# Kernel tuning notes

Measured on AMD Instinct MI355X. Metric: run time of the kernel, lower is better.

Reference implementation:

```python
import jax, jax.numpy as jnp
import numpy as np

B, N, C = 64, 8192, 64
C4 = C // 4
EPS_BN = 1e-5


def setup_inputs() -> dict:
    key = jax.random.key(0)
    ks = jax.random.split(key, 12)
    s = 0.05
    return {
        "x": jax.random.normal(ks[0], (B, N, 10), jnp.float32),
        "y": jax.random.normal(ks[1], (B, N, 13), jnp.float32),
        "W_l": jax.random.normal(ks[2], (10, C), jnp.float32) * s,
        "b_l": jax.random.normal(ks[3], (C,), jnp.float32) * s,
        "W_r": jax.random.normal(ks[4], (13, C), jnp.float32) * s,
        "b_r": jax.random.normal(ks[5], (C,), jnp.float32) * s,
        "W_qk": jax.random.normal(ks[6], (C4, C), jnp.float32) * s,  # shared q/k 1x1-conv weight
        "W_v": jax.random.normal(ks[7], (C, C), jnp.float32) * s,
        "b_v": jax.random.normal(ks[8], (C,), jnp.float32) * s,
        "W_t": jax.random.normal(ks[9], (C, C), jnp.float32) * s,
        "b_t": jax.random.normal(ks[10], (C,), jnp.float32) * s,
        "gamma": jnp.ones((C,), jnp.float32),
        "beta": jnp.zeros((C,), jnp.float32),
    }


def reference(x, y, W_l, b_l, W_r, b_r, W_qk, W_v, b_v, W_t, b_t, gamma, beta):
    # x: [B,N,10] -> linear_l; y: [B,N,13] -> linear_r  (torch keeps [B,C,N]; we keep [B,N,C])
    X = x @ W_l + b_l                                   # [B,N,C]
    Y = y @ W_r + b_r                                   # [B,N,C]
    # 1x1 convs == per-point matmuls; attention runs ACROSS the batch dim per point n
    xq = jnp.einsum('bnc,dc->nbd', X, W_qk)             # [N,B,C/4]
    yk = jnp.einsum('bnc,dc->nbd', Y, W_qk)             # [N,B,C/4] (shared weight)
    yv = jnp.einsum('bnc,dc->nbd', Y, W_v) + b_v        # [N,B,C]
    energy = jnp.einsum('nbd,ned->nbe', xq, yk)         # [N,B,B]
    attn = jax.nn.softmax(energy, axis=-1)
    # extra L1 renormalization over dim=1 (offset-attention style)
    attn = attn / (1e-9 + attn.sum(axis=1, keepdims=True))
    yr = jnp.einsum('nbe,nec->bnc', attn, yv)           # [B,N,C]
    # trans_conv -> BatchNorm (training-mode batch stats) -> ReLU -> residual -> max over points
    t = jnp.einsum('bnc,dc->bnd', X - yr, W_t) + b_t    # [B,N,C]
    mean = t.mean(axis=(0, 1))
    var = t.var(axis=(0, 1))                            # biased var, as BN uses
    tn = gamma * (t - mean) * jax.lax.rsqrt(var + EPS_BN) + beta
    xres = X + jax.nn.relu(tn)                          # [B,N,C]
    return jnp.max(xres, axis=1)[:, :, None]            # [B,C,1] to match torch layout
```

## Files before the change

### kernel.cpp

```cpp
#include <hip/hip_runtime.h>

#define B_ 64
#define N_ 8192

using short8 = __attribute__((ext_vector_type(8))) short;
using f32x4  = __attribute__((ext_vector_type(4))) float;

#define MFMA16(a, b, c) __builtin_amdgcn_mfma_f32_16x16x32_bf16((a), (b), (c), 0, 0, 0)

__device__ inline unsigned short f2bf(float f) {
  union { float f; unsigned int u; } v; v.f = f;
  return (unsigned short)((v.u + 0x8000u) >> 16);
}
__device__ inline float bf2f(unsigned int hi16_in_low) {
  union { unsigned int u; float f; } v; v.u = hi16_in_low << 16;
  return v.f;
}
__device__ inline unsigned u2(float a, float b) {
  return (unsigned)f2bf(a) | ((unsigned)f2bf(b) << 16);
}
__device__ inline void put_y(short* Ar0, short* YT0, int b, int f, unsigned short h) {
  const int s = (f >= 13) ? 1 : 0;
  Ar0[16 + f + 2547 * s] = (short)h;
  YT0[f * 72 + b + 216 * s] = (short)h;
}


__global__ void k0_prep(const float* __restrict__ W_l, const float* __restrict__ b_l,
                        const float* __restrict__ W_r, const float* __restrict__ b_r,
                        const float* __restrict__ W_qk, const float* __restrict__ W_v,
                        const float* __restrict__ b_v, const float* __restrict__ W_t,
                        float* __restrict__ wsf) {
  const int tid = threadIdx.x;
  unsigned short* wb   = (unsigned short*)(wsf + 66688);
  unsigned short* BM   = wb;
  unsigned short* BL   = wb + 512;
  unsigned short* BRV2 = wb + 2560;
  unsigned short* BT   = wb + 4608;
  if (blockIdx.x == 0) {
    __shared__ float Wlq[11 * 16], Wrk[14 * 16];
    for (int idx = tid; idx < 11 * 16; idx += 256) {
      int i = idx >> 4, d = idx & 15;
      const float* a = (i < 10) ? (W_l + i * 64) : b_l;
      float s = 0.f;
      for (int c = 0; c < 64; ++c) s = fmaf(a[c], W_qk[d * 64 + c], s);
      Wlq[idx] = s;
    }
    for (int idx = tid; idx < 14 * 16; idx += 256) {
      int j = idx >> 4, d = idx & 15;
      const float* a = (j < 13) ? (W_r + j * 64) : b_r;
      float s = 0.f;
      for (int c = 0; c < 64; ++c) s = fmaf(a[c], W_qk[d * 64 + c], s);
      Wrk[idx] = s;
    }
    __syncthreads();
    for (int idx = tid; idx < 512; idx += 256) {
      int j = idx >> 5, kk = idx & 31;
      unsigned short o = 0;
      if (j < 14 && kk < 11) {
        float s = 0.f;
        for (int d = 0; d < 16; ++d) s = fmaf(Wlq[kk * 16 + d], Wrk[j * 16 + d], s);
        o = f2bf(s);
      }
      BM[idx] = o;
    }
  } else if (blockIdx.x == 1) {
    for (int idx = tid; idx < 2048; idx += 256) {
      int c = idx >> 5, kk = idx & 31;
      unsigned short o = 0;
      if (kk < 13) {
        float s = 0.f;
        for (int j = 0; j < 64; ++j) s = fmaf(W_r[kk * 64 + j], W_v[c * 64 + j], s);
        o = f2bf(s);
      } else if (kk == 13) {
        float s = b_v[c];
        for (int j = 0; j < 64; ++j) s = fmaf(b_r[j], W_v[c * 64 + j], s);
        o = f2bf(s);
      }
      BRV2[idx] = o;
    }
  } else if (blockIdx.x == 2) {
    for (int idx = tid; idx < 2048; idx += 256) {
      int c = idx >> 5, kk = idx & 31;
      unsigned short o = 0;
      if (kk < 10) o = f2bf(W_l[kk * 64 + c]);
      else if (kk == 10) o = f2bf(b_l[c]);
      BL[idx] = o;
    }
    for (int i = tid; i < 1024; i += 256) wsf[i] = 0.f;
  } else {
    for (int i = tid; i < 4096; i += 256) BT[i] = f2bf(W_t[i]);
  }
}

__global__ __launch_bounds__(256, 4)
void k1_attn(const float* __restrict__ x, const float* __restrict__ y,
             const float* __restrict__ wsf, const float* __restrict__ b_t,
             float* __restrict__ stats) {
  __shared__ __align__(16) short lds[19712];
  float* const statsScr = (float*)lds;
  short* const Axy[2] = {lds, lds + 2560};
  short* const YTb[2] = {lds + 5120, lds + 6272};
  short* const awB    = lds + 7424;
  short* const guB    = lds + 16640;
  float* const csF    = (float*)(lds + 18688);

  const unsigned short* wb   = (const unsigned short*)(wsf + 66688);
  const unsigned short* BM   = wb;
  const unsigned short* BL   = wb + 512;
  const unsigned short* BRV2 = wb + 2560;
  const unsigned short* BT   = wb + 4608;
  unsigned short* tg = (unsigned short*)(wsf + 66688) + 8704;

  const int tid  = threadIdx.x;
  const int w    = tid >> 6;
  const int lane = tid & 63;
  const int l15  = lane & 15;
  const int q    = lane >> 4;
  const int r0   = w * 16;
  const int n0   = blockIdx.x * 2;
  short* const aw[2] = {awB + w * 1152, awB + (4 + w) * 1152};
  short* const gu[2] = {guB + w * 256,  guB + (4 + w) * 256};

  {
    const int b = tid >> 2, i = tid & 3;
    const float* xb = x + ((size_t)b * N_ + n0) * 10;
    const float* yb = y + ((size_t)b * N_ + n0) * 13;
    short* const Ar0 = Axy[0] + b * 40;
    short* const Ar1 = Axy[1] + b * 40;
    short* const YT0 = YTb[0];
    {
      const float4 v = *(const float4*)(xb + 4 * i);
      const int g0 = 4 * i, g1 = 4 * i + 2;
      *(unsigned*)(Ar0 + (g0 >= 10 ? g0 + 2550 : g0)) = u2(v.x, v.y);
      *(unsigned*)(Ar0 + (g1 >= 10 ? g1 + 2550 : g1)) = u2(v.z, v.w);
      if (i == 0) {
        const float4 vv = *(const float4*)(xb + 16);
        *(unsigned*)(Ar1 + 6) = u2(vv.x, vv.y);
        *(unsigned*)(Ar1 + 8) = u2(vv.z, vv.w);
      }
    }
    if (i == 1) { *(unsigned*)(Ar1 + 10) = 0x3F80u; *(unsigned*)(Ar1 + 12) = 0u; *(unsigned*)(Ar1 + 14) = 0u; }
    if (i == 2) { *(unsigned*)(Ar0 + 10) = 0x3F80u; *(unsigned*)(Ar0 + 12) = 0u; *(unsigned*)(Ar0 + 14) = 0u; }
#pragma unroll
    for (int t = 0; t < 3; ++t) {
      const int j = i + 4 * t;
      const float2 v = *(const float2*)(yb + 2 * j);
      put_y(Ar0, YT0, b, 2 * j,     f2bf(v.x));
      put_y(Ar0, YT0, b, 2 * j + 1, f2bf(v.y));
    }
    if (i == 0) {
      const float2 v = *(const float2*)(yb + 24);
      put_y(Ar0, YT0, b, 24, f2bf(v.x));
      put_y(Ar0, YT0, b, 25, f2bf(v.y));
    }
    if (i == 3) {
      Ar0[29] = (short)0x3F80; *(unsigned*)(Ar0 + 30) = 0u;
      YT0[13 * 72 + b] = (short)0x3F80; YT0[14 * 72 + b] = 0; YT0[15 * 72 + b] = 0;
    }
    if (i == 2) {
      Ar1[29] = (short)0x3F80; *(unsigned*)(Ar1 + 30) = 0u;
      short* YT1 = YT0 + 1152;
      YT1[13 * 72 + b] = (short)0x3F80; YT1[14 * 72 + b] = 0; YT1[15 * 72 + b] = 0;
    }
  }
  asm volatile("s_waitcnt lgkmcnt(0)" ::: "memory");
  __builtin_amdgcn_sched_barrier(0);

  const short8 z8 = {0, 0, 0, 0, 0, 0, 0, 0};
  const f32x4 zero4 = {0.f, 0.f, 0.f, 0.f};

  const short8 bmF = *(const short8*)&BM[l15 * 32 + q * 8];
  short8 blF[4];
#pragma unroll
  for (int f = 0; f < 4; ++f) blF[f] = *(const short8*)&BL[(f * 16 + l15) * 32 + q * 8];

  f32x4 X[2][4];
  __builtin_amdgcn_s_setprio(1);
#pragma unroll
  for (int p = 0; p < 2; ++p) {
    const short8 aA = *(const short8*)&Axy[p][(r0 + l15) * 40 + q * 8];
    f32x4 G = MFMA16(aA, bmF, zero4);
#pragma unroll
    for (int f = 0; f < 4; ++f) X[p][f] = MFMA16(aA, blF[f], zero4);
#pragma unroll
    for (int j = 0; j < 4; ++j) gu[p][(q * 4 + j) * 16 + l15] = (short)f2bf(G[j]);
  }
  __builtin_amdgcn_s_setprio(0);
  __syncthreads();

  f32x4 E[2][4];
  __builtin_amdgcn_s_setprio(1);
#pragma unroll
  for (int p = 0; p < 2; ++p) {
    short8 aG = z8;
    if (q < 2) aG = *(const short8*)&gu[p][l15 * 16 + q * 8];
#pragma unroll
    for (int f = 0; f < 4; ++f) {
      short8 bk = z8;
      if (q < 2) bk = *(const short8*)&Axy[p][(f * 16 + l15) * 40 + 16 + q * 8];
      E[p][f] = MFMA16(aG, bk, zero4);
    }
  }
  __builtin_amdgcn_s_setprio(0);

  float inv_r[2][4];
#pragma unroll
  for (int p = 0; p < 2; ++p)
#pragma unroll
    for (int j = 0; j < 4; ++j) {
      float s = 0.f;
#pragma unroll
      for (int f = 0; f < 4; ++f) { E[p][f][j] = __expf(E[p][f][j]); s += E[p][f][j]; }
      s += __shfl_xor(s, 1);
      s += __shfl_xor(s, 2);
      s += __shfl_xor(s, 4);
      s += __shfl_xor(s, 8);
      inv_r[p][j] = 1.0f / s;
    }
#pragma unroll
  for (int p = 0; p < 2; ++p)
#pragma unroll
    for (int f = 0; f < 4; ++f) {
      float cs = E[p][f][0] * inv_r[p][0] + E[p][f][1] * inv_r[p][1] +
                 E[p][f][2] * inv_r[p][2] + E[p][f][3] * inv_r[p][3];
      cs += __shfl_xor(cs, 16);
      cs += __shfl_xor(cs, 32);
      if (lane < 16) csF[p * 256 + w * 64 + f * 16 + l15] = cs;
    }
  __syncthreads();

#pragma unroll
  for (int p = 0; p < 2; ++p) {
#pragma unroll
    for (int f = 0; f < 4; ++f) {
      const int col = f * 16 + l15;
      const float* sp = csF + p * 256;
      const float csv = 1.0f / (1e-9f + sp[col] + sp[64 + col] + sp[128 + col] + sp[192 + col]);
#pragma unroll
      for (int j = 0; j < 4; ++j)
        aw[p][(q * 4 + j) * 72 + col] = (short)f2bf(E[p][f][j] * inv_r[p][j] * csv);
    }
  }

  short8 brvF[4];
#pragma unroll
  for (int f = 0; f < 4; ++f) brvF[f] = *(const short8*)&BRV2[(f * 16 + l15) * 32 + q * 8];
  __builtin_amdgcn_s_setprio(1);
#pragma unroll
  for (int p = 0; p < 2; ++p) {
    const short8 aA0 = *(const short8*)&aw[p][l15 * 72 + q * 8];
    const short8 aA1 = *(const short8*)&aw[p][l15 * 72 + 32 + q * 8];
    f32x4 U = MFMA16(aA0, *(const short8*)&YTb[p][l15 * 72 + q * 8], zero4);
    U = MFMA16(aA1, *(const short8*)&YTb[p][l15 * 72 + 32 + q * 8], U);
#pragma unroll
    for (int j = 0; j < 4; ++j) gu[p][(q * 4 + j) * 16 + l15] = (short)f2bf(U[j]);
    short8 aU = z8;
    if (q < 2) aU = *(const short8*)&gu[p][l15 * 16 + q * 8];
#pragma unroll
    for (int f = 0; f < 4; ++f) {
      f32x4 yr = MFMA16(aU, brvF[f], zero4);
#pragma unroll
      for (int j = 0; j < 4; ++j)
        aw[p][(q * 4 + j) * 72 + f * 16 + l15] = (short)f2bf(X[p][f][j] - yr[j]);
    }
  }
  __builtin_amdgcn_s_setprio(0);

  float sRed[2][4], ssRed[2][4];
  uint2 pk[2][4];
  float4 btv[4];
  short8 btF0[4], btF1[4];
#pragma unroll
  for (int f = 0; f < 4; ++f) {
    btv[f] = *(const float4*)&b_t[f * 16 + q * 4];
    const int c = f * 16 + l15;
    btF0[f] = *(const short8*)&BT[c * 64 + q * 8];
    btF1[f] = *(const short8*)&BT[c * 64 + 32 + q * 8];
  }
  __builtin_amdgcn_s_setprio(1);
#pragma unroll
  for (int p = 0; p < 2; ++p) {
    const short8 aZ0 = *(const short8*)&aw[p][l15 * 72 + q * 8];
    const short8 aZ1 = *(const short8*)&aw[p][l15 * 72 + 32 + q * 8];
#pragma unroll
    for (int f = 0; f < 4; ++f) {
      const int c = f * 16 + l15;
      const float bT = b_t[c];
      f32x4 t = MFMA16(aZ0, btF0[f], ((f32x4){bT, bT, bT, bT}));
      t = MFMA16(aZ1, btF1[f], t);
      float s = 0.f, ss = 0.f;
#pragma unroll
      for (int j = 0; j < 4; ++j) { s += t[j]; ss = fmaf(t[j], t[j], ss); }
      s  += __shfl_xor(s, 16);  s  += __shfl_xor(s, 32);
      ss += __shfl_xor(ss, 16); ss += __shfl_xor(ss, 32);
      sRed[p][f] = s; ssRed[p][f] = ss;
      f32x4 tc = MFMA16(btF0[f], aZ0, ((f32x4){btv[f].x, btv[f].y, btv[f].z, btv[f].w}));
      tc = MFMA16(btF1[f], aZ1, tc);
      pk[p][f].x = (unsigned)f2bf(tc[0]) | ((unsigned)f2bf(tc[1]) << 16);
      pk[p][f].y = (unsigned)f2bf(tc[2]) | ((unsigned)f2bf(tc[3]) << 16);
    }
  }
  __builtin_amdgcn_s_setprio(0);
#pragma unroll
  for (int p = 0; p < 2; ++p)
#pragma unroll
    for (int f = 0; f < 4; ++f)
      *(uint2*)&tg[(size_t)(n0 + p) * 4096 + (size_t)(r0 + l15) * 64 + f * 16 + q * 4] =
          pk[p][f];
#pragma unroll
  for (int p = 0; p < 2; ++p)
#pragma unroll
    for (int f = 0; f < 4; ++f)
      if (lane < 16) {
        statsScr[p * 512 + w * 64 + f * 16 + l15]       = sRed[p][f];
        statsScr[p * 512 + 256 + w * 64 + f * 16 + l15] = ssRed[p][f];
      }
  __syncthreads();
  if (tid < 128) {
    const int p = tid >> 6, c = tid & 63;
    const float* sp = statsScr + p * 512;
    const float s  = sp[c] + sp[64 + c] + sp[128 + c] + sp[192 + c];
    const float ss = sp[256 + c] + sp[320 + c] + sp[384 + c] + sp[448 + c];
    float* st = stats + ((n0 + p) & 7) * 128;
    atomicAdd(&st[c], s);
    atomicAdd(&st[64 + c], ss);
  }
}

__global__ __launch_bounds__(256)
void k3_max(const float* __restrict__ x, const float* __restrict__ W_l,
            const float* __restrict__ b_l, const float* __restrict__ gamma,
            const float* __restrict__ beta, const unsigned short* __restrict__ tg,
            const float* __restrict__ stats, float* __restrict__ pmax)
{
  const int b = blockIdx.x >> 4;
  const int chunk = blockIdx.x & 15;
  __shared__ __align__(16) float xs[512 * 10];
  __shared__ float mr[128];
  __shared__ float sm[4][64];
  {
    const float4* src = (const float4*)(x + ((size_t)b * N_ + (size_t)chunk * 512) * 10);
    float4* dst = (float4*)xs;
#pragma unroll
    for (int t = 0; t < 5; ++t) dst[threadIdx.x + 256 * t] = src[threadIdx.x + 256 * t];
  }
  if (threadIdx.x < 64) {
    const int c = threadIdx.x;
    float s = 0.f, ss = 0.f;
    for (int r = 0; r < 8; ++r) { s += stats[r * 128 + c]; ss += stats[r * 128 + 64 + c]; }
    const float inv = 1.0f / (float)(B_ * N_);
    const float mu = s * inv;
    const float var = fmaf(ss, inv, -mu * mu);
    mr[c] = mu;
    mr[64 + c] = rsqrtf(var + 1e-5f);
  }
  const int wv = threadIdx.x >> 6;
  const int lane = threadIdx.x & 63;
  const int c0 = (lane & 15) * 4;
  const int nsub = lane >> 4;
  float4 wl4[10];
#pragma unroll
  for (int k = 0; k < 10; ++k) wl4[k] = *(const float4*)&W_l[k * 64 + c0];
  const float4 bl  = *(const float4*)&b_l[c0];
  const float4 g   = *(const float4*)&gamma[c0];
  const float4 be  = *(const float4*)&beta[c0];
  __syncthreads();
  const float4 mu  = *(const float4*)&mr[c0];
  const float4 rs  = *(const float4*)&mr[64 + c0];
  float4 grs, bmb;
  grs.x = g.x * rs.x; grs.y = g.y * rs.y; grs.z = g.z * rs.z; grs.w = g.w * rs.w;
  bmb.x = be.x - mu.x * grs.x; bmb.y = be.y - mu.y * grs.y;
  bmb.z = be.z - mu.z * grs.z; bmb.w = be.w - mu.w * grs.w;
  float4 m = {-1e30f, -1e30f, -1e30f, -1e30f};
  const int ln0 = wv * 128 + nsub;
  const size_t tgbase = (size_t)(chunk * 512) * 4096 + (b << 6) + c0;
  uint2 tv[4];
#pragma unroll
  for (int u = 0; u < 4; ++u)
    tv[u] = *(const uint2*)&tg[tgbase + (size_t)(ln0 + u * 4) * 4096];
  for (int blk = 0; blk < 8; ++blk) {
    uint2 cur[4];
#pragma unroll
    for (int u = 0; u < 4; ++u) cur[u] = tv[u];
    if (blk < 7) {
#pragma unroll
      for (int u = 0; u < 4; ++u)
        tv[u] = *(const uint2*)&tg[tgbase + (size_t)(ln0 + (blk + 1) * 16 + u * 4) * 4096];
    }
#pragma unroll
    for (int u = 0; u < 4; ++u) {
      const int ln = ln0 + blk * 16 + u * 4;
      const float2* xr = (const float2*)(xs + ln * 10);
      float4 X = bl;
#pragma unroll
      for (int k = 0; k < 5; ++k) {
        const float2 xk = xr[k];
        X.x = fmaf(xk.x, wl4[2 * k].x, X.x); X.y = fmaf(xk.x, wl4[2 * k].y, X.y);
        X.z = fmaf(xk.x, wl4[2 * k].z, X.z); X.w = fmaf(xk.x, wl4[2 * k].w, X.w);
        X.x = fmaf(xk.y, wl4[2 * k + 1].x, X.x); X.y = fmaf(xk.y, wl4[2 * k + 1].y, X.y);
        X.z = fmaf(xk.y, wl4[2 * k + 1].z, X.z); X.w = fmaf(xk.y, wl4[2 * k + 1].w, X.w);
      }
      const float t0 = bf2f(cur[u].x & 0xFFFFu), t1 = bf2f(cur[u].x >> 16);
      const float t2 = bf2f(cur[u].y & 0xFFFFu), t3 = bf2f(cur[u].y >> 16);
      m.x = fmaxf(m.x, X.x + fmaxf(fmaf(t0, grs.x, bmb.x), 0.f));
      m.y = fmaxf(m.y, X.y + fmaxf(fmaf(t1, grs.y, bmb.y), 0.f));
      m.z = fmaxf(m.z, X.z + fmaxf(fmaf(t2, grs.z, bmb.z), 0.f));
      m.w = fmaxf(m.w, X.w + fmaxf(fmaf(t3, grs.w, bmb.w), 0.f));
    }
  }
  m.x = fmaxf(m.x, __shfl_xor(m.x, 16)); m.y = fmaxf(m.y, __shfl_xor(m.y, 16));
  m.z = fmaxf(m.z, __shfl_xor(m.z, 16)); m.w = fmaxf(m.w, __shfl_xor(m.w, 16));
  m.x = fmaxf(m.x, __shfl_xor(m.x, 32)); m.y = fmaxf(m.y, __shfl_xor(m.y, 32));
  m.z = fmaxf(m.z, __shfl_xor(m.z, 32)); m.w = fmaxf(m.w, __shfl_xor(m.w, 32));
  if (lane < 16) *(float4*)&sm[wv][c0] = m;
  __syncthreads();
  if (threadIdx.x < 64) {
    const float r = fmaxf(fmaxf(sm[0][threadIdx.x], sm[1][threadIdx.x]),
                          fmaxf(sm[2][threadIdx.x], sm[3][threadIdx.x]));
    pmax[(size_t)blockIdx.x * 64 + threadIdx.x] = r;
  }
}

__global__ void k4_final(const float* __restrict__ pmax, float* __restrict__ out) {
  const int b = blockIdx.x, c = threadIdx.x;
  float m = -1e30f;
  for (int ch = 0; ch < 16; ++ch) m = fmaxf(m, pmax[((size_t)b * 16 + ch) * 64 + c]);
  out[b * 64 + c] = m;
}

extern "C" void kernel_launch(void* const* d_in, const int* in_sizes, int n_in,
                              void* d_out, int out_size, void* d_ws, size_t ws_size,
                              hipStream_t stream) {
  const float* x     = (const float*)d_in[0];
  const float* y     = (const float*)d_in[1];
  const float* W_l   = (const float*)d_in[2];
  const float* b_l   = (const float*)d_in[3];
  const float* W_r   = (const float*)d_in[4];
  const float* b_r   = (const float*)d_in[5];
  const float* W_qk  = (const float*)d_in[6];
  const float* W_v   = (const float*)d_in[7];
  const float* b_v   = (const float*)d_in[8];
  const float* W_t   = (const float*)d_in[9];
  const float* b_t   = (const float*)d_in[10];
  const float* gamma = (const float*)d_in[11];
  const float* beta  = (const float*)d_in[12];
  float* out = (float*)d_out;

  float* wsf = (float*)d_ws;
  float* stats = wsf;
  float* pmax  = wsf + 1152;
  const unsigned short* tg = (const unsigned short*)(wsf + 66688) + 8704;

  hipLaunchKernelGGL(k0_prep, dim3(4), dim3(256), 0, stream,
                     W_l, b_l, W_r, b_r, W_qk, W_v, b_v, W_t, wsf);
  hipLaunchKernelGGL(k1_attn, dim3(N_ / 2), dim3(256), 0, stream,
                     x, y, wsf, b_t, stats);
  hipLaunchKernelGGL(k3_max, dim3(1024), dim3(256), 0, stream,
                     x, W_l, b_l, gamma, beta, tg, stats, pmax);
  hipLaunchKernelGGL(k4_final, dim3(64), dim3(64), 0, stream, pmax, out);
}
```

Measured before the change: 203.2 us.

## Store t batch-major for contiguous max reads; fold final max into atomic last-block

The intermediate t buffer changes from point-major [N][B][C] to batch-major [B][N][C]. Each k3_max block now reads a contiguous run instead of rows strided 8 KB apart, while k1's writes become strided. The separate final-reduction kernel is removed. Per-block maxima are merged through an order-preserving unsigned atomicMax, and the last block, detected via an atomic counter, writes the output. This saves one launch but adds atomics and a threadfence.

Measured after the change: 278.8 us. +37.2%, slower.

```diff
diff --git a/kernel.cpp b/kernel.cpp
--- a/kernel.cpp
+++ b/kernel.cpp
@@ -18,6 +18,13 @@
 }
 __device__ inline unsigned u2(float a, float b) {
   return (unsigned)f2bf(a) | ((unsigned)f2bf(b) << 16);
+}
+__device__ inline unsigned fkey(float f) {
+  unsigned u = __float_as_uint(f);
+  return (u & 0x80000000u) ? ~u : (u | 0x80000000u);
+}
+__device__ inline float funkey(unsigned k) {
+  return (k & 0x80000000u) ? __uint_as_float(k ^ 0x80000000u) : __uint_as_float(~k);
 }
 __device__ inline void put_y(short* Ar0, short* YT0, int b, int f, unsigned short h) {
   const int s = (f >= 13) ? 1 : 0;
@@ -79,6 +86,8 @@
       }
       BRV2[idx] = o;
     }
+    unsigned* wu = (unsigned*)wsf;
+    for (int i = tid; i < 4097; i += 256) wu[2048 + i] = 0u;
   } else if (blockIdx.x == 2) {
     for (int idx = tid; idx < 2048; idx += 256) {
       int c = idx >> 5, kk = idx & 31;
@@ -306,7 +315,7 @@
   for (int p = 0; p < 2; ++p)
 #pragma unroll
     for (int f = 0; f < 4; ++f)
-      *(uint2*)&tg[(size_t)(n0 + p) * 4096 + (size_t)(r0 + l15) * 64 + f * 16 + q * 4] =
+      *(uint2*)&tg[(size_t)(r0 + l15) * (N_ * 64) + (size_t)(n0 + p) * 64 + f * 16 + q * 4] =
           pk[p][f];
 #pragma unroll
   for (int p = 0; p < 2; ++p)
@@ -332,13 +341,15 @@
 void k3_max(const float* __restrict__ x, const float* __restrict__ W_l,
             const float* __restrict__ b_l, const float* __restrict__ gamma,
             const float* __restrict__ beta, const unsigned short* __restrict__ tg,
-            const float* __restrict__ stats, float* __restrict__ pmax)
+            const float* __restrict__ stats, unsigned* __restrict__ keys,
+            unsigned* __restrict__ cnt, float* __restrict__ out)
 {
   const int b = blockIdx.x >> 4;
   const int chunk = blockIdx.x & 15;
   __shared__ __align__(16) float xs[512 * 10];
   __shared__ float mr[128];
   __shared__ float sm[4][64];
+  __shared__ unsigned islast;
   {
     const float4* src = (const float4*)(x + ((size_t)b * N_ + (size_t)chunk * 512) * 10);
     float4* dst = (float4*)xs;
@@ -374,11 +385,11 @@
   bmb.z = be.z - mu.z * grs.z; bmb.w = be.w - mu.w * grs.w;
   float4 m = {-1e30f, -1e30f, -1e30f, -1e30f};
   const int ln0 = wv * 128 + nsub;
-  const size_t tgbase = (size_t)(chunk * 512) * 4096 + (b << 6) + c0;
+  const size_t tgbase = (size_t)b * (N_ * 64) + (size_t)(chunk * 512) * 64 + c0;
   uint2 tv[4];
 #pragma unroll
   for (int u = 0; u < 4; ++u)
-    tv[u] = *(const uint2*)&tg[tgbase + (size_t)(ln0 + u * 4) * 4096];
+    tv[u] = *(const uint2*)&tg[tgbase + (size_t)(ln0 + u * 4) * 64];
   for (int blk = 0; blk < 8; ++blk) {
     uint2 cur[4];
 #pragma unroll
@@ -386,7 +397,7 @@
     if (blk < 7) {
 #pragma unroll
       for (int u = 0; u < 4; ++u)
-        tv[u] = *(const uint2*)&tg[tgbase + (size_t)(ln0 + (blk + 1) * 16 + u * 4) * 4096];
+        tv[u] = *(const uint2*)&tg[tgbase + (size_t)(ln0 + (blk + 1) * 16 + u * 4) * 64];
     }
 #pragma unroll
     for (int u = 0; u < 4; ++u) {
@@ -418,15 +429,16 @@
   if (threadIdx.x < 64) {
     const float r = fmaxf(fmaxf(sm[0][threadIdx.x], sm[1][threadIdx.x]),
                           fmaxf(sm[2][threadIdx.x], sm[3][threadIdx.x]));
-    pmax[(size_t)blockIdx.x * 64 + threadIdx.x] = r;
-  }
-}
-
-__global__ void k4_final(const float* __restrict__ pmax, float* __restrict__ out) {
-  const int b = blockIdx.x, c = threadIdx.x;
-  float m = -1e30f;
-  for (int ch = 0; ch < 16; ++ch) m = fmaxf(m, pmax[((size_t)b * 16 + ch) * 64 + c]);
-  out[b * 64 + c] = m;
+    atomicMax(&keys[b * 64 + threadIdx.x], fkey(r));
+  }
+  __threadfence();
+  if (threadIdx.x == 0)
+    islast = (atomicAdd(cnt, 1u) == (unsigned)(gridDim.x - 1)) ? 1u : 0u;
+  __syncthreads();
+  if (islast) {
+    for (int i = threadIdx.x; i < 4096; i += 256)
+      out[i] = funkey(atomicOr(&keys[i], 0u));
+  }
 }
 
 extern "C" void kernel_launch(void* const* d_in, const int* in_sizes, int n_in,
@@ -449,7 +461,8 @@
 
   float* wsf = (float*)d_ws;
   float* stats = wsf;
-  float* pmax  = wsf + 1152;
+  unsigned* keys = (unsigned*)(wsf + 2048);
+  unsigned* cnt  = (unsigned*)(wsf + 6144);
   const unsigned short* tg = (const unsigned short*)(wsf + 66688) + 8704;
 
   hipLaunchKernelGGL(k0_prep, dim3(4), dim3(256), 0, stream,
@@ -457,6 +470,5 @@
   hipLaunchKernelGGL(k1_attn, dim3(N_ / 2), dim3(256), 0, stream,
                      x, y, wsf, b_t, stats);
   hipLaunchKernelGGL(k3_max, dim3(1024), dim3(256), 0, stream,
-                     x, W_l, b_l, gamma, beta, tg, stats, pmax);
-  hipLaunchKernelGGL(k4_final, dim3(64), dim3(64), 0, stream, pmax, out);
-}
+                     x, W_l, b_l, gamma, beta, tg, stats, keys, cnt, out);
+}
```
